# Performance work log

Measured on AMD Instinct MI355X. Metric: run time of the kernel, lower is better.

The kernel has to match this reference:

```python
import jax, jax.numpy as jnp
import numpy as np

B = 4        # number of point clouds (equal-size contiguous batches)
P = 8192     # points per cloud
C_IN = 64
C_OUT = 64
K = 16       # kNN neighbors (includes the point itself, as in PyG knn)
EPS = 1e-5
NEG_SLOPE = 0.2


def setup_inputs() -> dict:
    key = jax.random.key(0)
    k1, k2, k3 = jax.random.split(key, 3)
    x = jax.random.normal(k1, (B * P, C_IN), dtype=jnp.float32)
    batch = jnp.repeat(jnp.arange(B, dtype=jnp.int64), P)  # sorted, equal sizes
    W = jax.random.normal(k2, (2 * C_IN, C_OUT), dtype=jnp.float32) * (1.0 / np.sqrt(2 * C_IN))
    b = jax.random.normal(k3, (C_OUT,), dtype=jnp.float32) * 0.01
    gamma = jnp.ones((C_OUT,), dtype=jnp.float32)
    beta = jnp.zeros((C_OUT,), dtype=jnp.float32)
    return {"x": x, "batch": batch, "W": W, "b": b, "gamma": gamma, "beta": beta}


def _edgeconv(x, W, b, gamma, beta):
    xb = x.reshape(B, P, C_IN)
    # per-cloud pairwise squared distances: [B, P, P]
    sq = jnp.sum(xb * xb, axis=-1)
    d = sq[:, :, None] + sq[:, None, :] - 2.0 * jnp.einsum("bpc,bqc->bpq", xb, xb)
    # k nearest neighbors (smallest distance, self included)
    _, idx = jax.lax.top_k(-d, K)                      # [B, P, K]
    xj = jax.vmap(lambda pts, ind: pts[ind])(xb, idx)  # [B, P, K, C_IN]
    xi = xb[:, :, None, :]
    e = jnp.concatenate([jnp.broadcast_to(xi, xj.shape), xj - xi], axis=-1)  # [B,P,K,2C]
    # edge MLP: Linear -> BatchNorm1d (training-mode batch stats over all edges) -> LeakyReLU
    h = jnp.einsum("bpke,eo->bpko", e, W) + b          # [B, P, K, C_OUT]
    hf = h.reshape(-1, C_OUT)
    mean = jnp.mean(hf, axis=0)
    var = jnp.mean(hf * hf, axis=0) - mean * mean      # biased variance (torch BN)
    hn = (h - mean) * jax.lax.rsqrt(var + EPS) * gamma + beta
    a = jnp.where(hn >= 0, hn, NEG_SLOPE * hn)
    # max aggregation over neighbors
    return jnp.max(a, axis=2).reshape(B * P, C_OUT)


def reference(x, batch, W, b, gamma, beta):
    # `batch` encodes B equal-size contiguous clouds; kNN is computed per cloud.
    return _edgeconv(x, W, b, gamma, beta)
```

## Files before the change

kernel.cpp:

```cpp
#include <hip/hip_runtime.h>
#include <cfloat>

#define BATCH 4
#define P 8192
#define C 64
#define KNN 16
#define NPTS (BATCH * P)
#define NEDGE (NPTS * KNN)
#define EPSV 1e-5f
#define SLOPE 0.2f
#define NQ 2
#define QCOLS (P / NQ)
#define NPART 4

typedef __attribute__((ext_vector_type(8))) short bf16x8;
typedef __attribute__((ext_vector_type(16))) float f32x16;


__device__ __forceinline__ unsigned short f2bf(float f) {
    unsigned u = __float_as_uint(f);
    u += 0x7FFFu + ((u >> 16) & 1u);
    return (unsigned short)(u >> 16);
}
__device__ __forceinline__ float bf2f(unsigned short s) {
    return __uint_as_float(((unsigned)s) << 16);
}

__global__ void prep_frag(const float* __restrict__ x, uint4* __restrict__ xfh,
                          uint4* __restrict__ xfm, uint4* __restrict__ xfl,
                          float* __restrict__ sq) {
    __shared__ float part[32][9];
    int tid = threadIdx.x;
    int ptl = tid >> 3, j8 = tid & 7;
    int g = blockIdx.x;
    int p = g * 32 + ptl;
    const float4* xp = (const float4*)(x + (size_t)p * C + j8 * 8);
    float4 a = xp[0], b = xp[1];
    float v[8] = {a.x, a.y, a.z, a.w, b.x, b.y, b.z, b.w};
    unsigned short hs[8], ms[8], ls[8];
    float ssum = 0.f;
#pragma unroll
    for (int e = 0; e < 8; ++e) {
        float xv = v[e];
        ssum = fmaf(xv, xv, ssum);
        unsigned short h = f2bf(xv);
        float r1 = xv - bf2f(h);
        unsigned short m = f2bf(r1);
        float r2 = r1 - bf2f(m);
        unsigned short l = f2bf(r2);
        hs[e] = h; ms[e] = m; ls[e] = l;
    }
    int dst = (g * 4 + (j8 >> 1)) * 64 + ptl + 32 * (j8 & 1);
    uint4 ph, pm, pl;
    ph.x = (unsigned)hs[0] | ((unsigned)hs[1] << 16);
    ph.y = (unsigned)hs[2] | ((unsigned)hs[3] << 16);
    ph.z = (unsigned)hs[4] | ((unsigned)hs[5] << 16);
    ph.w = (unsigned)hs[6] | ((unsigned)hs[7] << 16);
    pm.x = (unsigned)ms[0] | ((unsigned)ms[1] << 16);
    pm.y = (unsigned)ms[2] | ((unsigned)ms[3] << 16);
    pm.z = (unsigned)ms[4] | ((unsigned)ms[5] << 16);
    pm.w = (unsigned)ms[6] | ((unsigned)ms[7] << 16);
    pl.x = (unsigned)ls[0] | ((unsigned)ls[1] << 16);
    pl.y = (unsigned)ls[2] | ((unsigned)ls[3] << 16);
    pl.z = (unsigned)ls[4] | ((unsigned)ls[5] << 16);
    pl.w = (unsigned)ls[6] | ((unsigned)ls[7] << 16);
    xfh[dst] = ph; xfm[dst] = pm; xfl[dst] = pl;
    part[ptl][j8] = ssum;
    __syncthreads();
    if (j8 == 0) {
        float s = 0.f;
#pragma unroll
        for (int k = 0; k < 8; ++k) s += part[ptl][k];
        sq[p] = s;
    }
}

__global__ __launch_bounds__(256, 4) void knn_kernel(const uint4* __restrict__ xfh,
                                                     const uint4* __restrict__ xfm,
                                                     const uint4* __restrict__ xfl,
                                                     const float* __restrict__ sq,
                                                     float* __restrict__ pv,
                                                     int* __restrict__ pi) {
    __shared__ float          bufv[4 * 32 * 33];
    __shared__ unsigned short bufi[4 * 32 * 33];
    __shared__ int            idL [4 * 32 * 17];
    __shared__ int            cntL[4 * 32];
    __shared__ float          worstL[4 * 32];

    int tid = threadIdx.x;
    int b = blockIdx.x & 3;
    int t = blockIdx.x >> 2;
    int tile = t & 127;
    int half = t >> 7;
    int bglob = b * P;
    int r0 = tile * 64;
    int colbase = half * QCOLS;
    int w = tid >> 6, lane = tid & 63;
    int wr = w & 1, wc = w >> 1;

    float*          bufvW = bufv + w * (32 * 33);
    unsigned short* bufiW = bufi + w * (32 * 33);
    int*            idLW  = idL  + w * (32 * 17);
    int*            cntW  = cntL + w * 32;
    float*          worstW = worstL + w * 32;

    if (lane < 32) { cntW[lane] = 0; worstW[lane] = FLT_MAX; }

    int gA = ((bglob + r0) >> 5) + wr;
    bf16x8 Ah[4], Am[4], Al[4];
#pragma unroll
    for (int kk = 0; kk < 4; ++kk) {
        Ah[kk] = __builtin_bit_cast(bf16x8, xfh[(gA * 4 + kk) * 64 + lane]);
        Am[kk] = __builtin_bit_cast(bf16x8, xfm[(gA * 4 + kk) * 64 + lane]);
        Al[kk] = __builtin_bit_cast(bf16x8, xfl[(gA * 4 + kk) * 64 + lane]);
    }

    float tv[16];
    float worst = FLT_MAX;
#pragma unroll
    for (int j = 0; j < 16; ++j) tv[j] = FLT_MAX;

    int rlbase = 4 * (lane >> 5);
    int sub = lane & 31;
    int colq = wc * 32 + sub;

    for (int chunk = 0; chunk < QCOLS / 64; ++chunk) {
        int c0 = colbase + chunk * 64;
        int gB = ((bglob + c0) >> 5) + wc;
        float sc = sq[bglob + c0 + colq];

        f32x16 acc;
#pragma unroll
        for (int i = 0; i < 16; ++i) acc[i] = 0.f;

        {
            bf16x8 Bh0 = __builtin_bit_cast(bf16x8, xfh[(gB * 4 + 0) * 64 + lane]);
            bf16x8 Bm0 = __builtin_bit_cast(bf16x8, xfm[(gB * 4 + 0) * 64 + lane]);
            bf16x8 Bl0 = __builtin_bit_cast(bf16x8, xfl[(gB * 4 + 0) * 64 + lane]);
            bf16x8 Bh1 = __builtin_bit_cast(bf16x8, xfh[(gB * 4 + 1) * 64 + lane]);
            bf16x8 Bm1 = __builtin_bit_cast(bf16x8, xfm[(gB * 4 + 1) * 64 + lane]);
            bf16x8 Bl1 = __builtin_bit_cast(bf16x8, xfl[(gB * 4 + 1) * 64 + lane]);
            acc = __builtin_amdgcn_mfma_f32_32x32x16_bf16(Ah[0], Bh0, acc, 0, 0, 0);
            acc = __builtin_amdgcn_mfma_f32_32x32x16_bf16(Am[0], Bh0, acc, 0, 0, 0);
            acc = __builtin_amdgcn_mfma_f32_32x32x16_bf16(Al[0], Bh0, acc, 0, 0, 0);
            acc = __builtin_amdgcn_mfma_f32_32x32x16_bf16(Ah[0], Bm0, acc, 0, 0, 0);
            acc = __builtin_amdgcn_mfma_f32_32x32x16_bf16(Am[0], Bm0, acc, 0, 0, 0);
            acc = __builtin_amdgcn_mfma_f32_32x32x16_bf16(Ah[0], Bl0, acc, 0, 0, 0);
            acc = __builtin_amdgcn_mfma_f32_32x32x16_bf16(Ah[1], Bh1, acc, 0, 0, 0);
            acc = __builtin_amdgcn_mfma_f32_32x32x16_bf16(Am[1], Bh1, acc, 0, 0, 0);
            acc = __builtin_amdgcn_mfma_f32_32x32x16_bf16(Al[1], Bh1, acc, 0, 0, 0);
            acc = __builtin_amdgcn_mfma_f32_32x32x16_bf16(Ah[1], Bm1, acc, 0, 0, 0);
            acc = __builtin_amdgcn_mfma_f32_32x32x16_bf16(Am[1], Bm1, acc, 0, 0, 0);
            acc = __builtin_amdgcn_mfma_f32_32x32x16_bf16(Ah[1], Bl1, acc, 0, 0, 0);
        }
        __builtin_amdgcn_sched_barrier(0);
        {
            bf16x8 Bh2 = __builtin_bit_cast(bf16x8, xfh[(gB * 4 + 2) * 64 + lane]);
            bf16x8 Bm2 = __builtin_bit_cast(bf16x8, xfm[(gB * 4 + 2) * 64 + lane]);
            bf16x8 Bl2 = __builtin_bit_cast(bf16x8, xfl[(gB * 4 + 2) * 64 + lane]);
            bf16x8 Bh3 = __builtin_bit_cast(bf16x8, xfh[(gB * 4 + 3) * 64 + lane]);
            bf16x8 Bm3 = __builtin_bit_cast(bf16x8, xfm[(gB * 4 + 3) * 64 + lane]);
            bf16x8 Bl3 = __builtin_bit_cast(bf16x8, xfl[(gB * 4 + 3) * 64 + lane]);
            acc = __builtin_amdgcn_mfma_f32_32x32x16_bf16(Ah[2], Bh2, acc, 0, 0, 0);
            acc = __builtin_amdgcn_mfma_f32_32x32x16_bf16(Am[2], Bh2, acc, 0, 0, 0);
            acc = __builtin_amdgcn_mfma_f32_32x32x16_bf16(Al[2], Bh2, acc, 0, 0, 0);
            acc = __builtin_amdgcn_mfma_f32_32x32x16_bf16(Ah[2], Bm2, acc, 0, 0, 0);
            acc = __builtin_amdgcn_mfma_f32_32x32x16_bf16(Am[2], Bm2, acc, 0, 0, 0);
            acc = __builtin_amdgcn_mfma_f32_32x32x16_bf16(Ah[2], Bl2, acc, 0, 0, 0);
            acc = __builtin_amdgcn_mfma_f32_32x32x16_bf16(Ah[3], Bh3, acc, 0, 0, 0);
            acc = __builtin_amdgcn_mfma_f32_32x32x16_bf16(Am[3], Bh3, acc, 0, 0, 0);
            acc = __builtin_amdgcn_mfma_f32_32x32x16_bf16(Al[3], Bh3, acc, 0, 0, 0);
            acc = __builtin_amdgcn_mfma_f32_32x32x16_bf16(Ah[3], Bm3, acc, 0, 0, 0);
            acc = __builtin_amdgcn_mfma_f32_32x32x16_bf16(Am[3], Bm3, acc, 0, 0, 0);
            acc = __builtin_amdgcn_mfma_f32_32x32x16_bf16(Ah[3], Bl3, acc, 0, 0, 0);
        }

        if (chunk == 0) {
#pragma unroll
            for (int reg = 0; reg < 16; ++reg) {
                float s = fmaf(-2.f, acc[reg], sc);
                int rl = rlbase + (reg & 3) + 8 * (reg >> 2);
                bufvW[rl * 33 + sub] = s;
            }
        } else {
            float4 twA[4];
#pragma unroll
            for (int g4 = 0; g4 < 4; ++g4)
                twA[g4] = *(const float4*)&worstW[rlbase + 8 * g4];
#pragma unroll
            for (int reg = 0; reg < 16; ++reg) {
                float s = fmaf(-2.f, acc[reg], sc);
                float tW = ((const float*)&twA[reg >> 2])[reg & 3];
                if (s < tW) {
                    int rl = rlbase + (reg & 3) + 8 * (reg >> 2);
                    int slot = atomicAdd(&cntW[rl], 1);
                    bufvW[rl * 33 + slot] = s;
                    bufiW[rl * 33 + slot] = (unsigned short)sub;
                }
            }
        }

        if (lane < 32) {
            int n = (chunk == 0) ? 32 : cntW[lane];
            int base = lane * 33;
            int id0 = bglob + c0 + wc * 32;
            for (int k = 0; k < n; ++k) {
                float s = bufvW[base + k];
                if (s < worst) {
                    float mx = tv[0];
                    int pos = 0;
#pragma unroll
                    for (int j = 1; j < 16; ++j) {
                        bool g = tv[j] > mx;
                        mx = g ? tv[j] : mx;
                        pos = g ? j : pos;
                    }
#pragma unroll
                    for (int j = 0; j < 16; ++j)
                        if (j == pos) tv[j] = s;
                    idLW[lane * 17 + pos] = (chunk == 0) ? (id0 + k)
                                                         : (id0 + (int)bufiW[base + k]);
                    float nw = fmaxf(fmaxf(fmaxf(tv[0], tv[1]), fmaxf(tv[2], tv[3])),
                                     fmaxf(fmaxf(tv[4], tv[5]), fmaxf(tv[6], tv[7])));
                    nw = fmaxf(nw, fmaxf(fmaxf(fmaxf(tv[8], tv[9]), fmaxf(tv[10], tv[11])),
                                         fmaxf(fmaxf(tv[12], tv[13]), fmaxf(tv[14], tv[15]))));
                    worst = nw;
                }
            }
            if (n > 0) { cntW[lane] = 0; worstW[lane] = worst; }
        }
    }

    if (lane < 32) {
        int qq = half * 2 + wc;
        size_t o = (((size_t)(bglob + r0 + wr * 32 + lane)) * NPART + qq) * KNN;
#pragma unroll
        for (int j = 0; j < 16; ++j) {
            pv[o + j] = tv[j];
            pi[o + j] = idLW[lane * 17 + j];
        }
    }
}

__global__ void merge_kernel(const float* __restrict__ pv, const int* __restrict__ pi,
                             int* __restrict__ idx_out) {
    __shared__ float mv[64][65];
    __shared__ int   mi[64][65];
    int tid = threadIdx.x;
    int lr = tid & 63, q = tid >> 6;
    int row = blockIdx.x * 64 + lr;
    size_t o = ((size_t)row * NPART + q) * KNN;
#pragma unroll
    for (int j = 0; j < 16; ++j) {
        mv[lr][q * 16 + j] = pv[o + j];
        mi[lr][q * 16 + j] = pi[o + j];
    }
    __syncthreads();
    if (tid < 64) {
        float tv[16];
        int ti[16];
        float worst = FLT_MAX;
#pragma unroll
        for (int j = 0; j < 16; ++j) { tv[j] = FLT_MAX; ti[j] = 0; }
        for (int e = 0; e < 64; ++e) {
            float s = mv[tid][e];
            if (s < worst) {
                float mx = tv[0];
                int pos = 0;
#pragma unroll
                for (int j = 1; j < 16; ++j) {
                    bool g = tv[j] > mx;
                    mx = g ? tv[j] : mx;
                    pos = g ? j : pos;
                }
#pragma unroll
                for (int j = 0; j < 16; ++j)
                    if (j == pos) { tv[j] = s; ti[j] = mi[tid][e]; }
                float nw = tv[0];
#pragma unroll
                for (int j = 1; j < 16; ++j) nw = fmaxf(nw, tv[j]);
                worst = nw;
            }
        }
        size_t oo = (size_t)row * KNN;
#pragma unroll
        for (int j = 0; j < 16; ++j) idx_out[oo + j] = ti[j];
    }
}

__global__ void prep_UV(const float* __restrict__ x, const float* __restrict__ W,
                        float* __restrict__ U, float* __restrict__ V) {
    __shared__ float Ws[128][64];
    __shared__ float xs[4][64];
    int tid = threadIdx.x;
    for (int i = tid; i < 128 * 64; i += 256) ((float*)Ws)[i] = W[i];
    int p0 = blockIdx.x * 4;
    int r = tid >> 6, c = tid & 63;
    xs[r][c] = x[(size_t)(p0 + r) * C + c];
    __syncthreads();
    float u = 0.f, v = 0.f;
#pragma unroll
    for (int k = 0; k < 64; ++k) {
        float xv = xs[r][k];
        float w1 = Ws[k][c];
        float w2 = Ws[64 + k][c];
        u = fmaf(xv, w1 - w2, u);
        v = fmaf(xv, w2, v);
    }
    size_t o = (size_t)(p0 + r) * C + c;
    U[o] = u;
    V[o] = v;
}

__global__ void stats_kernel(const float* __restrict__ U, const float* __restrict__ V,
                             const float* __restrict__ bias, const int* __restrict__ idx,
                             float* __restrict__ stats, float* __restrict__ Vmx,
                             float* __restrict__ Vmn) {
    int tid = threadIdx.x;
    int c = tid & 63, g = tid >> 6;
    int p0 = blockIdx.x * 16;
    float bc = bias[c];
    float sum = 0.f, sumsq = 0.f;
    for (int pp = g; pp < 16; pp += 4) {
        int p = p0 + pp;
        float u = U[(size_t)p * C + c] + bc;
        float mx = -FLT_MAX, mn = FLT_MAX;
#pragma unroll
        for (int k = 0; k < KNN; ++k) {
            int j = idx[(size_t)p * KNN + k];
            float v = V[(size_t)j * C + c];
            mx = fmaxf(mx, v);
            mn = fminf(mn, v);
            float h = u + v;
            sum += h;
            sumsq = fmaf(h, h, sumsq);
        }
        Vmx[(size_t)p * C + c] = mx;
        Vmn[(size_t)p * C + c] = mn;
    }
    __shared__ float red[2][4][64];
    red[0][g][c] = sum;
    red[1][g][c] = sumsq;
    __syncthreads();
    if (tid < 64) {
        float s = red[0][0][tid] + red[0][1][tid] + red[0][2][tid] + red[0][3][tid];
        atomicAdd(&stats[tid], s);
    } else if (tid < 128) {
        int cc = tid - 64;
        float s = red[1][0][cc] + red[1][1][cc] + red[1][2][cc] + red[1][3][cc];
        atomicAdd(&stats[64 + cc], s);
    }
}

__global__ void finalize_kernel(const float* __restrict__ stats,
                                const float* __restrict__ gamma,
                                const float* __restrict__ beta,
                                float* __restrict__ sshift) {
    int c = threadIdx.x;
    const float N = (float)NEDGE;
    float mean = stats[c] / N;
    float var = stats[64 + c] / N - mean * mean;
    float s = gamma[c] * rsqrtf(var + EPSV);
    sshift[c] = s;
    sshift[64 + c] = beta[c] - mean * s;
}

__global__ void out_kernel(const float* __restrict__ U, const float* __restrict__ bias,
                           const float* __restrict__ sshift, const float* __restrict__ Vmx,
                           const float* __restrict__ Vmn, float* __restrict__ out) {
    int i = (blockIdx.x * 256 + threadIdx.x) * 4;
    int c = i & 63;
    float4 sv = *(const float4*)&sshift[c];
    float4 tv = *(const float4*)&sshift[64 + c];
    float4 bb = *(const float4*)&bias[c];
    float4 u  = *(const float4*)&U[i];
    float4 mx = *(const float4*)&Vmx[i];
    float4 mn = *(const float4*)&Vmn[i];
    float4 r;
    {
        float hsel = (sv.x >= 0.f) ? mx.x : mn.x;
        float hn = fmaf(sv.x, u.x + bb.x + hsel, tv.x);
        r.x = (hn >= 0.f) ? hn : SLOPE * hn;
    }
    {
        float hsel = (sv.y >= 0.f) ? mx.y : mn.y;
        float hn = fmaf(sv.y, u.y + bb.y + hsel, tv.y);
        r.y = (hn >= 0.f) ? hn : SLOPE * hn;
    }
    {
        float hsel = (sv.z >= 0.f) ? mx.z : mn.z;
        float hn = fmaf(sv.z, u.z + bb.z + hsel, tv.z);
        r.z = (hn >= 0.f) ? hn : SLOPE * hn;
    }
    {
        float hsel = (sv.w >= 0.f) ? mx.w : mn.w;
        float hn = fmaf(sv.w, u.w + bb.w + hsel, tv.w);
        r.w = (hn >= 0.f) ? hn : SLOPE * hn;
    }
    *(float4*)&out[i] = r;
}

extern "C" void kernel_launch(void* const* d_in, const int* in_sizes, int n_in,
                              void* d_out, int out_size, void* d_ws, size_t ws_size,
                              hipStream_t stream) {
    const float* x     = (const float*)d_in[0];
    const float* W     = (const float*)d_in[2];
    const float* bias  = (const float*)d_in[3];
    const float* gamma = (const float*)d_in[4];
    const float* beta  = (const float*)d_in[5];
    float* out = (float*)d_out;

    float* wsf    = (float*)d_ws;
    float* U      = wsf;
    float* V      = wsf + 2097152;
    uint4* xfh    = (uint4*)wsf;
    uint4* xfm    = (uint4*)(wsf + 1048576);
    uint4* xfl    = (uint4*)(wsf + 2097152);
    float* sq     = wsf + 4194304;
    float* stats  = wsf + 4227072;
    float* sshift = wsf + 4227200;
    int*   idx    = (int*)(wsf + 4227328);
    float* pv     = wsf + 4751616;
    int*   pi     = (int*)(wsf + 6848768);
    float* Vmx    = wsf + 4751616;
    float* Vmn    = wsf + 6848768;

    hipLaunchKernelGGL(prep_frag, dim3(NPTS / 32), dim3(256), 0, stream, x, xfh, xfm, xfl, sq);
    hipLaunchKernelGGL(knn_kernel, dim3(BATCH * (P / 64) * NQ), dim3(256), 0, stream,
                       (const uint4*)xfh, (const uint4*)xfm, (const uint4*)xfl, sq, pv, pi);
    hipLaunchKernelGGL(merge_kernel, dim3(NPTS / 64), dim3(256), 0, stream, pv, pi, idx);
    hipLaunchKernelGGL(prep_UV, dim3(NPTS / 4), dim3(256), 0, stream, x, W, U, V);
    hipMemsetAsync(stats, 0, 128 * sizeof(float), stream);
    hipLaunchKernelGGL(stats_kernel, dim3(NPTS / 16), dim3(256), 0, stream, U, V, bias, idx,
                       stats, Vmx, Vmn);
    hipLaunchKernelGGL(finalize_kernel, dim3(1), dim3(64), 0, stream, stats, gamma, beta, sshift);
    hipLaunchKernelGGL(out_kernel, dim3(NPTS * C / 1024), dim3(256), 0, stream,
                       U, bias, sshift, Vmx, Vmn, out);
}
```

Measured before the change: 597.3 us.

## Vectorize kNN candidate buffer reads and amortize W staging in UV prep

The kNN candidate buffers get a row stride of 36 so each lane can read candidate distances and indices four at a time with vector LDS loads instead of scalar loads. prep_UV now handles 16 points per block instead of 4, which amortizes staging the 128x64 weight matrix into shared memory, and it precomputes W1-W2 once in shared memory. stats_kernel processes 32 points per block to cut block count and atomic reductions. The changes add padding and bounds checks inside the vector loop, and larger blocks mean fewer blocks to fill the GPU.

Result: no change. 586.6 us (-1.8%).

```diff
diff --git a/kernel.cpp b/kernel.cpp
--- a/kernel.cpp
+++ b/kernel.cpp
@@ -12,6 +12,7 @@
 #define NQ 2
 #define QCOLS (P / NQ)
 #define NPART 4
+#define BSTR 36
 
 typedef __attribute__((ext_vector_type(8))) short bf16x8;
 typedef __attribute__((ext_vector_type(16))) float f32x16;
@@ -81,8 +82,8 @@
                                                      const float* __restrict__ sq,
                                                      float* __restrict__ pv,
                                                      int* __restrict__ pi) {
-    __shared__ float          bufv[4 * 32 * 33];
-    __shared__ unsigned short bufi[4 * 32 * 33];
+    __shared__ float          bufv[4 * 32 * BSTR];
+    __shared__ unsigned short bufi[4 * 32 * BSTR];
     __shared__ int            idL [4 * 32 * 17];
     __shared__ int            cntL[4 * 32];
     __shared__ float          worstL[4 * 32];
@@ -98,8 +99,8 @@
     int w = tid >> 6, lane = tid & 63;
     int wr = w & 1, wc = w >> 1;
 
-    float*          bufvW = bufv + w * (32 * 33);
-    unsigned short* bufiW = bufi + w * (32 * 33);
+    float*          bufvW = bufv + w * (32 * BSTR);
+    unsigned short* bufiW = bufi + w * (32 * BSTR);
     int*            idLW  = idL  + w * (32 * 17);
     int*            cntW  = cntL + w * 32;
     float*          worstW = worstL + w * 32;
@@ -180,7 +181,7 @@
             for (int reg = 0; reg < 16; ++reg) {
                 float s = fmaf(-2.f, acc[reg], sc);
                 int rl = rlbase + (reg & 3) + 8 * (reg >> 2);
-                bufvW[rl * 33 + sub] = s;
+                bufvW[rl * BSTR + sub] = s;
             }
         } else {
             float4 twA[4];
@@ -194,37 +195,48 @@
                 if (s < tW) {
                     int rl = rlbase + (reg & 3) + 8 * (reg >> 2);
                     int slot = atomicAdd(&cntW[rl], 1);
-                    bufvW[rl * 33 + slot] = s;
-                    bufiW[rl * 33 + slot] = (unsigned short)sub;
+                    bufvW[rl * BSTR + slot] = s;
+                    bufiW[rl * BSTR + slot] = (unsigned short)sub;
                 }
             }
         }
 
         if (lane < 32) {
+            int base = lane * BSTR;
+            int id0 = bglob + c0 + wc * 32;
             int n = (chunk == 0) ? 32 : cntW[lane];
-            int base = lane * 33;
-            int id0 = bglob + c0 + wc * 32;
-            for (int k = 0; k < n; ++k) {
-                float s = bufvW[base + k];
-                if (s < worst) {
-                    float mx = tv[0];
-                    int pos = 0;
-#pragma unroll
-                    for (int j = 1; j < 16; ++j) {
-                        bool g = tv[j] > mx;
-                        mx = g ? tv[j] : mx;
-                        pos = g ? j : pos;
+            for (int k0 = 0; k0 < n; k0 += 4) {
+                float4 s4 = *(const float4*)&bufvW[base + k0];
+                ushort4 i4;
+                if (chunk != 0) i4 = *(const ushort4*)&bufiW[base + k0];
+                float sj[4] = {s4.x, s4.y, s4.z, s4.w};
+                unsigned short ij[4];
+                if (chunk != 0) { ij[0] = i4.x; ij[1] = i4.y; ij[2] = i4.z; ij[3] = i4.w; }
+#pragma unroll
+                for (int j = 0; j < 4; ++j) {
+                    if (k0 + j < n) {
+                        float s = sj[j];
+                        if (s < worst) {
+                            float mx = tv[0];
+                            int pos = 0;
+#pragma unroll
+                            for (int jj = 1; jj < 16; ++jj) {
+                                bool g = tv[jj] > mx;
+                                mx = g ? tv[jj] : mx;
+                                pos = g ? jj : pos;
+                            }
+#pragma unroll
+                            for (int jj = 0; jj < 16; ++jj)
+                                if (jj == pos) tv[jj] = s;
+                            idLW[lane * 17 + pos] = (chunk == 0) ? (id0 + k0 + j)
+                                                                 : (id0 + (int)ij[j]);
+                            float nw = fmaxf(fmaxf(fmaxf(tv[0], tv[1]), fmaxf(tv[2], tv[3])),
+                                             fmaxf(fmaxf(tv[4], tv[5]), fmaxf(tv[6], tv[7])));
+                            nw = fmaxf(nw, fmaxf(fmaxf(fmaxf(tv[8], tv[9]), fmaxf(tv[10], tv[11])),
+                                                 fmaxf(fmaxf(tv[12], tv[13]), fmaxf(tv[14], tv[15]))));
+                            worst = nw;
+                        }
                     }
-#pragma unroll
-                    for (int j = 0; j < 16; ++j)
-                        if (j == pos) tv[j] = s;
-                    idLW[lane * 17 + pos] = (chunk == 0) ? (id0 + k)
-                                                         : (id0 + (int)bufiW[base + k]);
-                    float nw = fmaxf(fmaxf(fmaxf(tv[0], tv[1]), fmaxf(tv[2], tv[3])),
-                                     fmaxf(fmaxf(tv[4], tv[5]), fmaxf(tv[6], tv[7])));
-                    nw = fmaxf(nw, fmaxf(fmaxf(fmaxf(tv[8], tv[9]), fmaxf(tv[10], tv[11])),
-                                         fmaxf(fmaxf(tv[12], tv[13]), fmaxf(tv[14], tv[15]))));
-                    worst = nw;
                 }
             }
             if (n > 0) { cntW[lane] = 0; worstW[lane] = worst; }
@@ -291,25 +303,28 @@
 __global__ void prep_UV(const float* __restrict__ x, const float* __restrict__ W,
                         float* __restrict__ U, float* __restrict__ V) {
     __shared__ float Ws[128][64];
-    __shared__ float xs[4][64];
+    __shared__ float xs[16][64];
     int tid = threadIdx.x;
     for (int i = tid; i < 128 * 64; i += 256) ((float*)Ws)[i] = W[i];
-    int p0 = blockIdx.x * 4;
+    int p0 = blockIdx.x * 16;
     int r = tid >> 6, c = tid & 63;
-    xs[r][c] = x[(size_t)(p0 + r) * C + c];
+    for (int rr = r; rr < 16; rr += 4) xs[rr][c] = x[(size_t)(p0 + rr) * C + c];
     __syncthreads();
-    float u = 0.f, v = 0.f;
-#pragma unroll
-    for (int k = 0; k < 64; ++k) {
-        float xv = xs[r][k];
-        float w1 = Ws[k][c];
-        float w2 = Ws[64 + k][c];
-        u = fmaf(xv, w1 - w2, u);
-        v = fmaf(xv, w2, v);
-    }
-    size_t o = (size_t)(p0 + r) * C + c;
-    U[o] = u;
-    V[o] = v;
+    for (int k = r * 16; k < r * 16 + 16; ++k)
+        Ws[k][c] = Ws[k][c] - Ws[64 + k][c];
+    __syncthreads();
+    for (int rr = r; rr < 16; rr += 4) {
+        float u = 0.f, v = 0.f;
+#pragma unroll
+        for (int k = 0; k < 64; ++k) {
+            float xv = xs[rr][k];
+            u = fmaf(xv, Ws[k][c], u);
+            v = fmaf(xv, Ws[64 + k][c], v);
+        }
+        size_t o = (size_t)(p0 + rr) * C + c;
+        U[o] = u;
+        V[o] = v;
+    }
 }
 
 __global__ void stats_kernel(const float* __restrict__ U, const float* __restrict__ V,
@@ -318,10 +333,10 @@
                              float* __restrict__ Vmn) {
     int tid = threadIdx.x;
     int c = tid & 63, g = tid >> 6;
-    int p0 = blockIdx.x * 16;
+    int p0 = blockIdx.x * 32;
     float bc = bias[c];
     float sum = 0.f, sumsq = 0.f;
-    for (int pp = g; pp < 16; pp += 4) {
+    for (int pp = g; pp < 32; pp += 4) {
         int p = p0 + pp;
         float u = U[(size_t)p * C + c] + bc;
         float mx = -FLT_MAX, mn = FLT_MAX;
@@ -429,9 +444,9 @@
     hipLaunchKernelGGL(knn_kernel, dim3(BATCH * (P / 64) * NQ), dim3(256), 0, stream,
                        (const uint4*)xfh, (const uint4*)xfm, (const uint4*)xfl, sq, pv, pi);
     hipLaunchKernelGGL(merge_kernel, dim3(NPTS / 64), dim3(256), 0, stream, pv, pi, idx);
-    hipLaunchKernelGGL(prep_UV, dim3(NPTS / 4), dim3(256), 0, stream, x, W, U, V);
+    hipLaunchKernelGGL(prep_UV, dim3(NPTS / 16), dim3(256), 0, stream, x, W, U, V);
     hipMemsetAsync(stats, 0, 128 * sizeof(float), stream);
-    hipLaunchKernelGGL(stats_kernel, dim3(NPTS / 16), dim3(256), 0, stream, U, V, bias, idx,
+    hipLaunchKernelGGL(stats_kernel, dim3(NPTS / 32), dim3(256), 0, stream, U, V, bias, idx,
                        stats, Vmx, Vmn);
     hipLaunchKernelGGL(finalize_kernel, dim3(1), dim3(64), 0, stream, stats, gamma, beta, sshift);
     hipLaunchKernelGGL(out_kernel, dim3(NPTS * C / 1024), dim3(256), 0, stream,
```
